# Optimization experiments

Measured on AMD Instinct MI355X. Metric: run time of the kernel, lower is better.

## Reference

```python
import jax, jax.numpy as jnp
import numpy as np

B, C, H, W = 8, 256, 64, 64
HEADS, HID = 8, 64
TMP = HEADS * HID  # 512


def setup_inputs() -> dict:
    key = jax.random.key(0)
    ks = jax.random.split(key, 6)
    s = lambda fan: 1.0 / np.sqrt(fan)
    fmap = jax.random.normal(ks[0], (B, C, H, W), jnp.float32)
    Wq = jax.random.normal(ks[1], (TMP, C), jnp.float32) * s(C)          # to_q 1x1 conv (no bias)
    Wdw = jax.random.normal(ks[2], (C, 1, 3, 3), jnp.float32) * s(9)     # depthwise 3x3 (groups=C, no bias)
    Wkv = jax.random.normal(ks[3], (2 * TMP, C), jnp.float32) * s(C)     # 1x1 conv producing k,v (no bias)
    Wout = jax.random.normal(ks[4], (C, TMP), jnp.float32) * s(TMP)      # to_out 1x1 conv
    bout = jax.random.normal(ks[5], (C,), jnp.float32) * 0.01
    return {"fmap": fmap, "Wq": Wq, "Wdw": Wdw, "Wkv": Wkv, "Wout": Wout, "bout": bout}


def reference(fmap, Wq, Wdw, Wkv, Wout, bout):
    heads, hid = HEADS, HID
    scale = hid ** (-0.5)
    b, c, h, w = fmap.shape
    n = h * w

    # 1x1 conv == channel GEMM
    q = jnp.einsum('bcxy,oc->boxy', fmap, Wq)
    # depthwise 3x3, padding=1
    dw = jax.lax.conv_general_dilated(
        fmap, Wdw, window_strides=(1, 1), padding='SAME',
        dimension_numbers=('NCHW', 'OIHW', 'NCHW'), feature_group_count=c)
    kv = jnp.einsum('bcxy,oc->boxy', dw, Wkv)
    k, v = jnp.split(kv, 2, axis=1)

    # 'b (h c) x y -> b h (x y) c'
    def to_seq(t):
        return t.reshape(b, heads, hid, n).transpose(0, 1, 3, 2)  # [b, h, n, d]

    q, k, v = to_seq(q), to_seq(k), to_seq(v)
    q = jax.nn.softmax(q, axis=-1) * scale   # softmax over feature dim
    k = jax.nn.softmax(k, axis=-2)           # softmax over token dim

    ctx = jnp.einsum('bhnd,bhne->bhde', k, v)    # [b, h, d, d]
    out = jnp.einsum('bhnd,bhde->bhne', q, ctx)  # [b, h, n, d]

    # '(b h) (x y) d -> b (h d) x y'
    out = out.transpose(0, 1, 3, 2).reshape(b, heads * hid, h, w)

    # to_out: GELU (exact) then 1x1 conv with bias (mode='ac')
    out = jax.nn.gelu(out, approximate=False)
    return jnp.einsum('bcxy,oc->boxy', out, Wout) + bout[None, :, None, None]
```

## Files before the change

kernel.cpp:

```cpp
#include <hip/hip_runtime.h>
#include <hip/hip_bf16.h>
#include <math.h>

#define Bx 8
#define Cc 256
#define Nn 4096
#define TMPc 512

typedef unsigned short ushort;
typedef unsigned int uint;
typedef unsigned long long ull;
typedef __attribute__((ext_vector_type(8))) short bf16x8;
typedef __attribute__((ext_vector_type(4))) float f32x4;

union F4 { float4 v; float f[4]; };

__device__ __forceinline__ ushort f2bf(float x) {
  uint u = __float_as_uint(x);
  uint r = (u + 0x7fffu + ((u >> 16) & 1u)) >> 16;
  return (ushort)r;
}
__device__ __forceinline__ float gelu_fast(float x) {
  float u = 0.70710678118654752f * x;
  float au = fabsf(u);
  float t = __builtin_amdgcn_rcpf(1.0f + 0.3275911f * au);
  float poly = ((((1.061405429f * t - 1.453152027f) * t + 1.421413741f) * t -
                 0.284496736f) * t + 0.254829592f) * t;
  float e = 1.0f - poly * __expf(-u * u);
  float erfu = copysignf(e, u);
  return 0.5f * x * (1.0f + erfu);
}

typedef const __attribute__((address_space(1))) uint* gp1_t;
typedef __attribute__((address_space(3))) uint* lp3_t;
__device__ __forceinline__ void gload16(void* lds, const void* g) {
  __builtin_amdgcn_global_load_lds((gp1_t)g, (lp3_t)lds, 16, 0, 0);
}
__device__ __forceinline__ bf16x8 fragread(const char* lds, int row, int kc) {
  return *(const bf16x8*)(lds + row * 64 + ((kc ^ (row & 3)) << 4));
}
__device__ __forceinline__ void stage2(char* buf, const ushort* src, int ld,
                                       int row0, int col, int w, int prow, int gst) {
  int off = __builtin_amdgcn_readfirstlane(w * 2048);
  gload16(buf + off, src + (size_t)(row0 + prow) * ld + col + gst * 8);
  gload16(buf + off + 1024, src + (size_t)(row0 + 16 + prow) * ld + col + gst * 8);
}

#define CGRP 32
__global__ __launch_bounds__(256) void convfuse_k(const float* __restrict__ fmap,
                                                  const float* __restrict__ Wdw,
                                                  ushort* __restrict__ fmapT,
                                                  ushort* __restrict__ dwT) {
  __shared__ float sin_[CGRP][6 * 64 + 1];
  __shared__ float wl[CGRP][9];
  int t = threadIdx.x;
  int y0 = blockIdx.x * 4;
  int c0 = blockIdx.y * CGRP;
  int z = blockIdx.z;
  for (int i = t; i < CGRP * 9; i += 256) wl[i / 9][i % 9] = Wdw[c0 * 9 + i];
  const float* src = fmap + ((size_t)z * Cc + c0) * 4096;
#pragma unroll
  for (int it = 0; it < 12; ++it) {
    int idx = it * 256 + t;
    int c = idx / 96, rem = idx % 96, yy = rem >> 4, x4 = rem & 15;
    int gy = y0 - 1 + yy;
    F4 v;
    if ((unsigned)gy < 64u)
      v.v = *(const float4*)&src[(size_t)c * 4096 + gy * 64 + x4 * 4];
    else
      v.f[0] = v.f[1] = v.f[2] = v.f[3] = 0.f;
#pragma unroll
    for (int j = 0; j < 4; ++j) sin_[c][yy * 64 + x4 * 4 + j] = v.f[j];
  }
  __syncthreads();
  int c8 = (t & 3) * 8;
  int nl = t >> 2;
  size_t nbase = (size_t)z * 4096 + (size_t)y0 * 64;
#pragma unroll
  for (int it = 0; it < 4; ++it) {
    int n = it * 64 + nl;
    int y = n >> 6, x = n & 63;
    union { ushort u[8]; uint4 q; } fo, go;
#pragma unroll
    for (int cc = 0; cc < 8; ++cc) {
      int c = c8 + cc;
      fo.u[cc] = f2bf(sin_[c][(y + 1) * 64 + x]);
      float acc = 0.f;
#pragma unroll
      for (int dy = 0; dy < 3; ++dy) {
#pragma unroll
        for (int dx = 0; dx < 3; ++dx) {
          int xx = x + dx - 1;
          float pv = ((unsigned)xx < 64u) ? sin_[c][(y + dy) * 64 + xx] : 0.f;
          acc += pv * wl[c][dy * 3 + dx];
        }
      }
      go.u[cc] = f2bf(acc);
    }
    *(uint4*)&fmapT[(nbase + n) * Cc + c0 + c8] = fo.q;
    *(uint4*)&dwT[(nbase + n) * Cc + c0 + c8] = go.q;
  }
}

__global__ __launch_bounds__(256) void cvtb3_k(const float* __restrict__ Wq,
                                               const float* __restrict__ Wkv,
                                               const float* __restrict__ Wout,
                                               ushort* __restrict__ WqB,
                                               ushort* __restrict__ WkvB,
                                               ushort* __restrict__ WoutB) {
  int i = blockIdx.x * 256 + threadIdx.x;
  const float* s;
  ushort* d;
  int idx;
  if (i < 32768) { s = Wq; d = WqB; idx = i; }
  else if (i < 98304) { s = Wkv; d = WkvB; idx = i - 32768; }
  else { s = Wout; d = WoutB; idx = i - 98304; }
  F4 v; v.v = *(const float4*)&s[(size_t)idx * 4];
  union { ushort u[4]; uint2 q; } o;
#pragma unroll
  for (int j = 0; j < 4; ++j) o.u[j] = f2bf(v.f[j]);
  *(uint2*)&d[(size_t)idx * 4] = o.q;
}

__global__ __launch_bounds__(256, 2) void kvgemm3_k(const ushort* __restrict__ WkvB,
                                                    const ushort* __restrict__ dwT,
                                                    ushort* __restrict__ kv) {
  __shared__ __align__(16) char lds[57344];
  char* Bres = lds;
  char* Asg  = lds + 32768;
  int t = threadIdx.x, w = t >> 6, l = t & 63;
  int z = blockIdx.y, n0 = blockIdx.x * 64;
  int rl = l & 15, kc = l >> 4;
  int prow = l >> 2;
  int gst = (l & 3) ^ ((l >> 2) & 3);

  const ushort* dT = dwT + ((size_t)z * 4096 + n0) * 256;
#pragma unroll
  for (int p = 0; p < 8; ++p) {
    int row = (w * 8 + p) * 2 + (l >> 5);
    int cs = l & 31;
    int off = __builtin_amdgcn_readfirstlane((w * 8 + p) * 1024);
    gload16(Bres + off, dT + (size_t)row * 256 + ((cs ^ (row & 7)) * 8));
  }
  stage2(Asg, WkvB, 256, w * 32, 0, w, prow, gst);
  stage2(Asg + 8192, WkvB, 256, w * 32, 32, w, prow, gst);
  asm volatile("s_waitcnt vmcnt(0)" ::: "memory");
  __syncthreads();

  ushort* kz = kv + (size_t)z * 1024 * 4096;
#pragma unroll
  for (int c = 0; c < 8; ++c) {
    f32x4 acc[2][4];
#pragma unroll
    for (int i = 0; i < 2; ++i)
#pragma unroll
      for (int j = 0; j < 4; ++j) acc[i][j] = (f32x4){0.f, 0.f, 0.f, 0.f};
#pragma unroll
    for (int k0 = 0; k0 < 8; ++k0) {
      int s = c * 8 + k0;
      if (s + 2 < 64) {
        int s2 = s + 2;
        stage2(Asg + (s2 % 3) * 8192, WkvB, 256, (s2 >> 3) * 128 + w * 32,
               (s2 & 7) * 32, w, prow, gst);
      }
      if (s < 62) asm volatile("s_waitcnt vmcnt(4)" ::: "memory");
      else if (s == 62) asm volatile("s_waitcnt vmcnt(2)" ::: "memory");
      else asm volatile("s_waitcnt vmcnt(0)" ::: "memory");
      const char* bp = Asg + (s % 3) * 8192 + w * 2048;
      bf16x8 a0 = fragread(bp, rl, kc);
      bf16x8 a1 = fragread(bp, 16 + rl, kc);
#pragma unroll
      for (int j = 0; j < 4; ++j) {
        int n = 16 * j + rl;
        bf16x8 b = *(const bf16x8*)(Bres + n * 512 + (((k0 * 4 + kc) ^ (n & 7)) << 4));
        acc[0][j] = __builtin_amdgcn_mfma_f32_16x16x32_bf16(a0, b, acc[0][j], 0, 0, 0);
        acc[1][j] = __builtin_amdgcn_mfma_f32_16x16x32_bf16(a1, b, acc[1][j], 0, 0, 0);
      }
    }
#pragma unroll
    for (int i = 0; i < 2; ++i) {
#pragma unroll
      for (int reg = 0; reg < 4; ++reg) {
        int r = c * 128 + w * 32 + 16 * i + 4 * kc + reg;
#pragma unroll
        for (int j = 0; j < 4; ++j) {
          int col = n0 + 16 * j + rl;
          float v = acc[i][j][reg];
          kz[(size_t)r * 4096 + col] = f2bf(c < 4 ? __expf(v) : v);
        }
      }
    }
  }
}

__global__ __launch_bounds__(256) void ctx_mfma(const ushort* __restrict__ kv,
                                                float* __restrict__ ctxf,
                                                float* __restrict__ sf) {
  __shared__ __align__(16) char lds[8192];
  int t = threadIdx.x, w = t >> 6, l = t & 63;
  int s = blockIdx.x;
  int h = blockIdx.y & 7, z = blockIdx.y >> 3;
  const ushort* kb = kv + ((size_t)z * 1024 + h * 64) * 4096;
  const ushort* vb = kv + ((size_t)z * 1024 + 512 + h * 64) * 4096;
  f32x4 acc[2][2];
  f32x4 accs[2];
#pragma unroll
  for (int i = 0; i < 2; ++i) {
    accs[i] = (f32x4){0.f, 0.f, 0.f, 0.f};
#pragma unroll
    for (int j = 0; j < 2; ++j) acc[i][j] = (f32x4){0.f, 0.f, 0.f, 0.f};
  }
  bf16x8 ones;
#pragma unroll
  for (int i = 0; i < 8; ++i) ones[i] = (short)0x3F80;
  int wr = (w >> 1) * 32, wc = (w & 1) * 32;
  int rl = l & 15, kc = l >> 4;
  int srow = (l >> 2) & 15, scol = l & 3;
  for (int it = 0; it < 16; ++it) {
    int k0 = s * 512 + it * 32;
    __syncthreads();
    {
      int row = w * 16 + srow;
      int g = scol ^ (row & 3);
      int off = __builtin_amdgcn_readfirstlane(w * 1024);
      gload16(lds + off, vb + (size_t)row * 4096 + k0 + g * 8);
      gload16(lds + 4096 + off, kb + (size_t)row * 4096 + k0 + g * 8);
    }
    asm volatile("s_waitcnt vmcnt(0)" ::: "memory");
    __syncthreads();
    bf16x8 a[2], b[2];
#pragma unroll
    for (int i = 0; i < 2; ++i) a[i] = fragread(lds, wr + i * 16 + rl, kc);
#pragma unroll
    for (int i = 0; i < 2; ++i) b[i] = fragread(lds + 4096, wc + i * 16 + rl, kc);
#pragma unroll
    for (int i = 0; i < 2; ++i)
#pragma unroll
      for (int j = 0; j < 2; ++j)
        acc[i][j] = __builtin_amdgcn_mfma_f32_16x16x32_bf16(a[i], b[j], acc[i][j], 0, 0, 0);
    if (w < 2) {
#pragma unroll
      for (int j = 0; j < 2; ++j)
        accs[j] = __builtin_amdgcn_mfma_f32_16x16x32_bf16(b[j], ones, accs[j], 0, 0, 0);
    }
  }
  float* cf = ctxf + (size_t)(z * 8 + h) * 4096;
#pragma unroll
  for (int i = 0; i < 2; ++i)
#pragma unroll
    for (int reg = 0; reg < 4; ++reg) {
      int e = wr + i * 16 + kc * 4 + reg;
#pragma unroll
      for (int j = 0; j < 2; ++j) {
        int d = wc + j * 16 + rl;
        atomicAdd(&cf[e * 64 + d], acc[i][j][reg]);
      }
    }
  if (w < 2 && rl == 0) {
    float* sp = sf + (size_t)(z * 8 + h) * 64;
#pragma unroll
    for (int j = 0; j < 2; ++j)
#pragma unroll
      for (int reg = 0; reg < 4; ++reg)
        atomicAdd(&sp[wc + j * 16 + kc * 4 + reg], accs[j][reg]);
  }
}

__global__ __launch_bounds__(256) void ctx_cvt(const float* __restrict__ ctxf,
                                               const float* __restrict__ sf,
                                               ushort* __restrict__ ctxb) {
  int page = blockIdx.x;
  const float* s = ctxf + (size_t)page * 4096;
  const float* sp = sf + (size_t)page * 64;
  ushort* d = ctxb + (size_t)page * 4096;
  int t = threadIdx.x;
  int e = t >> 2, d0 = (t & 3) * 16;
  union { ushort u[16]; uint4 q[2]; } o;
#pragma unroll
  for (int j = 0; j < 16; ++j) {
    int dd = d0 + j;
    o.u[j] = f2bf(s[e * 64 + dd] / sp[dd]);
  }
  uint4* dp = (uint4*)&d[e * 64 + d0];
  dp[0] = o.q[0]; dp[1] = o.q[1];
}

__global__ __launch_bounds__(256, 2) void qao_k(const ushort* __restrict__ fmapT,
                                                const ushort* __restrict__ WqB,
                                                const ushort* __restrict__ ctxb,
                                                const ushort* __restrict__ WoutB,
                                                const float* __restrict__ bout,
                                                float* __restrict__ out) {
  __shared__ __align__(16) char lds[73728];
  __shared__ float wsum[4][64];
  char* qbuf = lds;
  char* Bres = lds + 16384;
  char* Asg  = lds + 49152;
  int t = threadIdx.x, w = t >> 6, l = t & 63;
  int z = blockIdx.y, n0 = blockIdx.x * 64;
  int rl = l & 15, kc = l >> 4;
  int prow = l >> 2;
  int gst = (l & 3) ^ ((l >> 2) & 3);
  int hh = w >> 1;
  int wcn = (w & 1) * 32;

  const ushort* fT = fmapT + ((size_t)z * 4096 + n0) * 256;
#pragma unroll
  for (int p = 0; p < 8; ++p) {
    int row = (w * 8 + p) * 2 + (l >> 5);
    int cs = l & 31;
    int off = __builtin_amdgcn_readfirstlane((w * 8 + p) * 1024);
    gload16(Bres + off, fT + (size_t)row * 256 + ((cs ^ (row & 7)) * 8));
  }
  stage2(Asg, WqB, 256, w * 32, 0, w, prow, gst);
  stage2(Asg + 8192, WqB, 256, w * 32, 32, w, prow, gst);

  f32x4 oacc[4][4];
#pragma unroll
  for (int i = 0; i < 4; ++i)
#pragma unroll
    for (int j = 0; j < 4; ++j) oacc[i][j] = (f32x4){0.f, 0.f, 0.f, 0.f};

  asm volatile("s_waitcnt vmcnt(0)" ::: "memory");
  __syncthreads();

  for (int c = 0; c < 4; ++c) {
    const ushort* Wqc = WqB + (size_t)(c * 128) * 256;
    f32x4 qa[2][4];
#pragma unroll
    for (int i = 0; i < 2; ++i)
#pragma unroll
      for (int j = 0; j < 4; ++j) qa[i][j] = (f32x4){0.f, 0.f, 0.f, 0.f};
#pragma unroll
    for (int k0 = 0; k0 < 8; ++k0) {
      if (k0 + 2 < 8)
        stage2(Asg + ((k0 + 2) % 3) * 8192, Wqc, 256, w * 32, (k0 + 2) * 32, w, prow, gst);
      if (k0 < 6) asm volatile("s_waitcnt vmcnt(4)" ::: "memory");
      else if (k0 == 6) asm volatile("s_waitcnt vmcnt(2)" ::: "memory");
      else asm volatile("s_waitcnt vmcnt(0)" ::: "memory");
      const char* bp = Asg + (k0 % 3) * 8192 + w * 2048;
      bf16x8 a0 = fragread(bp, rl, kc);
      bf16x8 a1 = fragread(bp, 16 + rl, kc);
#pragma unroll
      for (int j = 0; j < 4; ++j) {
        int n = 16 * j + rl;
        bf16x8 b = *(const bf16x8*)(Bres + n * 512 + (((k0 * 4 + kc) ^ (n & 7)) << 4));
        qa[0][j] = __builtin_amdgcn_mfma_f32_16x16x32_bf16(a0, b, qa[0][j], 0, 0, 0);
        qa[1][j] = __builtin_amdgcn_mfma_f32_16x16x32_bf16(a1, b, qa[1][j], 0, 0, 0);
      }
    }
    const ushort* cpg = ctxb + (size_t)(z * 8 + c * 2 + hh) * 4096;
    bf16x8 ca[2][4];
#pragma unroll
    for (int s2 = 0; s2 < 2; ++s2)
#pragma unroll
      for (int i = 0; i < 4; ++i)
        ca[s2][i] = *(const bf16x8*)(cpg + (size_t)(16 * i + rl) * 64 + s2 * 32 + kc * 8);
    float sj[4];
#pragma unroll
    for (int j = 0; j < 4; ++j) {
      float s = 0.f;
#pragma unroll
      for (int i = 0; i < 2; ++i)
#pragma unroll
        for (int reg = 0; reg < 4; ++reg) {
          float e = __expf(qa[i][j][reg]);
          qa[i][j][reg] = e;
          s += e;
        }
      s += __shfl_xor(s, 16, 64);
      s += __shfl_xor(s, 32, 64);
      sj[j] = s;
    }
    if (l < 16) {
#pragma unroll
      for (int j = 0; j < 4; ++j) wsum[w][j * 16 + l] = sj[j];
    }
    __syncthreads();
#pragma unroll
    for (int j = 0; j < 4; ++j) {
      float tot = wsum[w][16 * j + rl] + wsum[w ^ 1][16 * j + rl];
      float inv = 0.125f / tot;
#pragma unroll
      for (int i = 0; i < 2; ++i)
#pragma unroll
        for (int reg = 0; reg < 4; ++reg) qa[i][j][reg] *= inv;
    }
#pragma unroll
    for (int i = 0; i < 2; ++i)
#pragma unroll
      for (int j = 0; j < 4; ++j) {
        int n = 16 * j + rl;
        int dby = (w * 32 + 16 * i + 4 * kc) * 2;
        union { ushort u[4]; ull q; } pk;
#pragma unroll
        for (int reg = 0; reg < 4; ++reg) pk.u[reg] = f2bf(qa[i][j][reg]);
        *(ull*)(qbuf + n * 256 + (dby ^ ((n & 7) << 4))) = pk.q;
      }
    __syncthreads();
    f32x4 pacc[4][2];
#pragma unroll
    for (int i = 0; i < 4; ++i)
#pragma unroll
      for (int j = 0; j < 2; ++j) pacc[i][j] = (f32x4){0.f, 0.f, 0.f, 0.f};
#pragma unroll
    for (int s2 = 0; s2 < 2; ++s2) {
      bf16x8 pb[2];
#pragma unroll
      for (int j = 0; j < 2; ++j) {
        int n = wcn + 16 * j + rl;
        int dby = hh * 128 + s2 * 64 + kc * 16;
        pb[j] = *(const bf16x8*)(qbuf + n * 256 + (dby ^ ((n & 7) << 4)));
      }
#pragma unroll
      for (int i = 0; i < 4; ++i)
#pragma unroll
        for (int j = 0; j < 2; ++j)
          pacc[i][j] = __builtin_amdgcn_mfma_f32_16x16x32_bf16(ca[s2][i], pb[j], pacc[i][j], 0, 0, 0);
    }
#pragma unroll
    for (int i = 0; i < 4; ++i)
#pragma unroll
      for (int j = 0; j < 2; ++j) {
        int n = wcn + 16 * j + rl;
        int mby = (hh * 64 + 16 * i + 4 * kc) * 2;
        union { ushort u[4]; ull q; } pk;
#pragma unroll
        for (int reg = 0; reg < 4; ++reg) pk.u[reg] = f2bf(gelu_fast(pacc[i][j][reg]));
        *(ull*)(qbuf + n * 256 + (mby ^ ((n & 7) << 4))) = pk.q;
      }
    __syncthreads();
    stage2(Asg, WoutB, 512, w * 64, c * 128, w, prow, gst);
    stage2(Asg + 8192, WoutB, 512, w * 64 + 32, c * 128, w, prow, gst);
    bf16x8 ob[4];
#pragma unroll
    for (int s = 0; s < 8; ++s) {
      if (s + 2 < 8) {
        int s2 = s + 2;
        stage2(Asg + (s2 % 3) * 8192, WoutB, 512, w * 64 + (s2 & 1) * 32,
               c * 128 + (s2 >> 1) * 32, w, prow, gst);
      }
      if (s < 6) asm volatile("s_waitcnt vmcnt(4)" ::: "memory");
      else if (s == 6) asm volatile("s_waitcnt vmcnt(2)" ::: "memory");
      else asm volatile("s_waitcnt vmcnt(0)" ::: "memory");
      int half = s & 1, ks = s >> 1;
      if (half == 0) {
#pragma unroll
        for (int j = 0; j < 4; ++j) {
          int n = 16 * j + rl;
          ob[j] = *(const bf16x8*)(qbuf + n * 256 + ((ks * 64 + kc * 16) ^ ((n & 7) << 4)));
        }
      }
      const char* bp = Asg + (s % 3) * 8192 + w * 2048;
      bf16x8 a0 = fragread(bp, rl, kc);
      bf16x8 a1 = fragread(bp, 16 + rl, kc);
#pragma unroll
      for (int j = 0; j < 4; ++j) {
        oacc[half * 2][j] = __builtin_amdgcn_mfma_f32_16x16x32_bf16(a0, ob[j], oacc[half * 2][j], 0, 0, 0);
        oacc[half * 2 + 1][j] = __builtin_amdgcn_mfma_f32_16x16x32_bf16(a1, ob[j], oacc[half * 2 + 1][j], 0, 0, 0);
      }
    }
    if (c < 3) {
      const ushort* Wqn = WqB + (size_t)((c + 1) * 128) * 256;
      stage2(Asg, Wqn, 256, w * 32, 0, w, prow, gst);
      stage2(Asg + 8192, Wqn, 256, w * 32, 32, w, prow, gst);
    }
  }
  float* oz = out + (size_t)z * Cc * Nn + n0;
#pragma unroll
  for (int i = 0; i < 4; ++i) {
#pragma unroll
    for (int reg = 0; reg < 4; ++reg) {
      int crow = w * 64 + 16 * i + 4 * kc + reg;
      float bv = bout[crow];
      float* rowp = oz + (size_t)crow * 4096;
#pragma unroll
      for (int j = 0; j < 4; ++j) rowp[16 * j + rl] = oacc[i][j][reg] + bv;
    }
  }
}

extern "C" void kernel_launch(void* const* d_in, const int* in_sizes, int n_in,
                              void* d_out, int out_size, void* d_ws, size_t ws_size,
                              hipStream_t stream) {
  (void)in_sizes; (void)n_in; (void)out_size; (void)ws_size;
  const float* fmap = (const float*)d_in[0];
  const float* Wq   = (const float*)d_in[1];
  const float* Wdw  = (const float*)d_in[2];
  const float* Wkv  = (const float*)d_in[3];
  const float* Wout = (const float*)d_in[4];
  const float* bout = (const float*)d_in[5];
  float* out = (float*)d_out;

  ushort* WqB   = (ushort*)d_ws;
  ushort* WkvB  = WqB + 512 * 256;
  ushort* WoutB = WkvB + 1024 * 256;
  ushort* fmapT = WoutB + 256 * 512;
  ushort* dwT   = fmapT + (size_t)Bx * 4096 * 256;
  ushort* kv    = dwT + (size_t)Bx * 4096 * 256;
  ushort* ctxb  = kv + (size_t)Bx * 1024 * 4096;
  float*  ctxf  = (float*)(ctxb + (size_t)Bx * 8 * 4096);
  float*  sf    = ctxf + (size_t)Bx * 8 * 64 * 64;

  cvtb3_k<<<dim3(512), 256, 0, stream>>>(Wq, Wkv, Wout, WqB, WkvB, WoutB);
  convfuse_k<<<dim3(16, Cc / CGRP, Bx), 256, 0, stream>>>(fmap, Wdw, fmapT, dwT);
  kvgemm3_k<<<dim3(64, Bx), 256, 0, stream>>>(WkvB, dwT, kv);
  hipMemsetAsync(ctxf, 0, (size_t)Bx * 8 * (4096 + 64) * sizeof(float), stream);
  ctx_mfma<<<dim3(8, Bx * 8), 256, 0, stream>>>(kv, ctxf, sf);
  ctx_cvt<<<dim3(Bx * 8), 256, 0, stream>>>(ctxf, sf, ctxb);
  qao_k<<<dim3(64, Bx), 256, 0, stream>>>(fmapT, WqB, ctxb, WoutB, bout, out);
}
```

Baseline: 122.4 us.

## Retile q/attention/out kernel to 32-token tiles with per-head loop for occupancy

The fused q-projection/attention/output kernel now processes 32 tokens per block instead of 64 and iterates over single heads rather than head pairs. That halves LDS use and accumulator registers so four blocks can share a CU, and the grid doubles to 128x8. It also adds lgkmcnt fences before LDS-overwriting async loads in the staging loops and moves the ctx memset to the start of the stream. In exchange, each block reloads the Wq and Wout weights for a smaller token tile, which raises weight traffic, and the per-head loop needs more barriers.

```diff
diff --git a/kernel.cpp b/kernel.cpp
--- a/kernel.cpp
+++ b/kernel.cpp
@@ -36,8 +36,16 @@
 __device__ __forceinline__ void gload16(void* lds, const void* g) {
   __builtin_amdgcn_global_load_lds((gp1_t)g, (lp3_t)lds, 16, 0, 0);
 }
+__device__ __forceinline__ void lgkm_fence() {
+  asm volatile("s_waitcnt lgkmcnt(0)" ::: "memory");
+}
 __device__ __forceinline__ bf16x8 fragread(const char* lds, int row, int kc) {
   return *(const bf16x8*)(lds + row * 64 + ((kc ^ (row & 3)) << 4));
+}
+__device__ __forceinline__ void stage1(char* buf, const ushort* src, int ld,
+                                       int row0, int col, int w, int prow, int gst) {
+  int off = __builtin_amdgcn_readfirstlane(w * 1024);
+  gload16(buf + off, src + (size_t)(row0 + prow) * ld + col + gst * 8);
 }
 __device__ __forceinline__ void stage2(char* buf, const ushort* src, int ld,
                                        int row0, int col, int w, int prow, int gst) {
@@ -160,6 +168,7 @@
       int s = c * 8 + k0;
       if (s + 2 < 64) {
         int s2 = s + 2;
+        lgkm_fence();
         stage2(Asg + (s2 % 3) * 8192, WkvB, 256, (s2 >> 3) * 128 + w * 32,
                (s2 & 7) * 32, w, prow, gst);
       }
@@ -285,197 +294,182 @@
   dp[0] = o.q[0]; dp[1] = o.q[1];
 }
 
-__global__ __launch_bounds__(256, 2) void qao_k(const ushort* __restrict__ fmapT,
+__global__ __launch_bounds__(256, 4) void qao_k(const ushort* __restrict__ fmapT,
                                                 const ushort* __restrict__ WqB,
                                                 const ushort* __restrict__ ctxb,
                                                 const ushort* __restrict__ WoutB,
                                                 const float* __restrict__ bout,
                                                 float* __restrict__ out) {
-  __shared__ __align__(16) char lds[73728];
-  __shared__ float wsum[4][64];
-  char* qbuf = lds;
-  char* Bres = lds + 16384;
-  char* Asg  = lds + 49152;
+  __shared__ __align__(16) char lds[36864];
+  __shared__ float wsum[4][32];
+  char* Bres = lds;
+  char* qB   = lds + 16384;
+  char* gB   = lds + 20480;
+  char* Asg  = lds + 24576;
   int t = threadIdx.x, w = t >> 6, l = t & 63;
-  int z = blockIdx.y, n0 = blockIdx.x * 64;
+  int z = blockIdx.y, n0 = blockIdx.x * 32;
   int rl = l & 15, kc = l >> 4;
   int prow = l >> 2;
   int gst = (l & 3) ^ ((l >> 2) & 3);
-  int hh = w >> 1;
-  int wcn = (w & 1) * 32;
+  int erow0 = w * 16;
+  int orow0 = w * 64;
 
   const ushort* fT = fmapT + ((size_t)z * 4096 + n0) * 256;
 #pragma unroll
-  for (int p = 0; p < 8; ++p) {
-    int row = (w * 8 + p) * 2 + (l >> 5);
+  for (int p = 0; p < 4; ++p) {
+    int row = (w * 4 + p) * 2 + (l >> 5);
     int cs = l & 31;
-    int off = __builtin_amdgcn_readfirstlane((w * 8 + p) * 1024);
+    int off = __builtin_amdgcn_readfirstlane((w * 4 + p) * 1024);
     gload16(Bres + off, fT + (size_t)row * 256 + ((cs ^ (row & 7)) * 8));
   }
-  stage2(Asg, WqB, 256, w * 32, 0, w, prow, gst);
-  stage2(Asg + 8192, WqB, 256, w * 32, 32, w, prow, gst);
-
-  f32x4 oacc[4][4];
-#pragma unroll
-  for (int i = 0; i < 4; ++i)
-#pragma unroll
-    for (int j = 0; j < 4; ++j) oacc[i][j] = (f32x4){0.f, 0.f, 0.f, 0.f};
+  stage1(Asg, WqB, 256, erow0, 0, w, prow, gst);
+  stage1(Asg + 4096, WqB, 256, erow0, 32, w, prow, gst);
+
+  f32x4 oacc[4][2];
+#pragma unroll
+  for (int g = 0; g < 4; ++g)
+#pragma unroll
+    for (int j = 0; j < 2; ++j) oacc[g][j] = (f32x4){0.f, 0.f, 0.f, 0.f};
 
   asm volatile("s_waitcnt vmcnt(0)" ::: "memory");
   __syncthreads();
 
-  for (int c = 0; c < 4; ++c) {
-    const ushort* Wqc = WqB + (size_t)(c * 128) * 256;
-    f32x4 qa[2][4];
-#pragma unroll
-    for (int i = 0; i < 2; ++i)
-#pragma unroll
-      for (int j = 0; j < 4; ++j) qa[i][j] = (f32x4){0.f, 0.f, 0.f, 0.f};
+  for (int h = 0; h < 8; ++h) {
+    const ushort* Wqc = WqB + (size_t)(h * 64) * 256;
+    f32x4 qa[2];
+#pragma unroll
+    for (int j = 0; j < 2; ++j) qa[j] = (f32x4){0.f, 0.f, 0.f, 0.f};
 #pragma unroll
     for (int k0 = 0; k0 < 8; ++k0) {
-      if (k0 + 2 < 8)
-        stage2(Asg + ((k0 + 2) % 3) * 8192, Wqc, 256, w * 32, (k0 + 2) * 32, w, prow, gst);
-      if (k0 < 6) asm volatile("s_waitcnt vmcnt(4)" ::: "memory");
-      else if (k0 == 6) asm volatile("s_waitcnt vmcnt(2)" ::: "memory");
+      if (k0 + 2 < 8) {
+        lgkm_fence();
+        stage1(Asg + ((k0 + 2) % 3) * 4096, Wqc, 256, erow0, (k0 + 2) * 32, w, prow, gst);
+      }
+      if (k0 < 6) asm volatile("s_waitcnt vmcnt(2)" ::: "memory");
+      else if (k0 == 6) asm volatile("s_waitcnt vmcnt(1)" ::: "memory");
       else asm volatile("s_waitcnt vmcnt(0)" ::: "memory");
-      const char* bp = Asg + (k0 % 3) * 8192 + w * 2048;
+      const char* bp = Asg + (k0 % 3) * 4096 + w * 1024;
       bf16x8 a0 = fragread(bp, rl, kc);
-      bf16x8 a1 = fragread(bp, 16 + rl, kc);
-#pragma unroll
-      for (int j = 0; j < 4; ++j) {
+#pragma unroll
+      for (int j = 0; j < 2; ++j) {
         int n = 16 * j + rl;
         bf16x8 b = *(const bf16x8*)(Bres + n * 512 + (((k0 * 4 + kc) ^ (n & 7)) << 4));
-        qa[0][j] = __builtin_amdgcn_mfma_f32_16x16x32_bf16(a0, b, qa[0][j], 0, 0, 0);
-        qa[1][j] = __builtin_amdgcn_mfma_f32_16x16x32_bf16(a1, b, qa[1][j], 0, 0, 0);
-      }
-    }
-    const ushort* cpg = ctxb + (size_t)(z * 8 + c * 2 + hh) * 4096;
-    bf16x8 ca[2][4];
+        qa[j] = __builtin_amdgcn_mfma_f32_16x16x32_bf16(a0, b, qa[j], 0, 0, 0);
+      }
+    }
+    const ushort* cpg = ctxb + (size_t)(z * 8 + h) * 4096;
+    bf16x8 ca[2];
 #pragma unroll
     for (int s2 = 0; s2 < 2; ++s2)
-#pragma unroll
-      for (int i = 0; i < 4; ++i)
-        ca[s2][i] = *(const bf16x8*)(cpg + (size_t)(16 * i + rl) * 64 + s2 * 32 + kc * 8);
-    float sj[4];
-#pragma unroll
-    for (int j = 0; j < 4; ++j) {
+      ca[s2] = *(const bf16x8*)(cpg + (size_t)(erow0 + rl) * 64 + s2 * 32 + kc * 8);
+    float sj[2];
+#pragma unroll
+    for (int j = 0; j < 2; ++j) {
       float s = 0.f;
 #pragma unroll
-      for (int i = 0; i < 2; ++i)
-#pragma unroll
-        for (int reg = 0; reg < 4; ++reg) {
-          float e = __expf(qa[i][j][reg]);
-          qa[i][j][reg] = e;
-          s += e;
-        }
+      for (int reg = 0; reg < 4; ++reg) {
+        float e = __expf(qa[j][reg]);
+        qa[j][reg] = e;
+        s += e;
+      }
       s += __shfl_xor(s, 16, 64);
       s += __shfl_xor(s, 32, 64);
       sj[j] = s;
     }
     if (l < 16) {
 #pragma unroll
-      for (int j = 0; j < 4; ++j) wsum[w][j * 16 + l] = sj[j];
+      for (int j = 0; j < 2; ++j) wsum[w][j * 16 + l] = sj[j];
     }
     __syncthreads();
 #pragma unroll
-    for (int j = 0; j < 4; ++j) {
-      float tot = wsum[w][16 * j + rl] + wsum[w ^ 1][16 * j + rl];
+    for (int j = 0; j < 2; ++j) {
+      float tot = wsum[0][16 * j + rl] + wsum[1][16 * j + rl] +
+                  wsum[2][16 * j + rl] + wsum[3][16 * j + rl];
       float inv = 0.125f / tot;
 #pragma unroll
-      for (int i = 0; i < 2; ++i)
-#pragma unroll
-        for (int reg = 0; reg < 4; ++reg) qa[i][j][reg] *= inv;
-    }
-#pragma unroll
-    for (int i = 0; i < 2; ++i)
-#pragma unroll
-      for (int j = 0; j < 4; ++j) {
-        int n = 16 * j + rl;
-        int dby = (w * 32 + 16 * i + 4 * kc) * 2;
-        union { ushort u[4]; ull q; } pk;
-#pragma unroll
-        for (int reg = 0; reg < 4; ++reg) pk.u[reg] = f2bf(qa[i][j][reg]);
-        *(ull*)(qbuf + n * 256 + (dby ^ ((n & 7) << 4))) = pk.q;
-      }
+      for (int reg = 0; reg < 4; ++reg) qa[j][reg] *= inv;
+    }
+#pragma unroll
+    for (int j = 0; j < 2; ++j) {
+      int n = 16 * j + rl;
+      int dby = (erow0 + 4 * kc) * 2;
+      union { ushort u[4]; ull q; } pk;
+#pragma unroll
+      for (int reg = 0; reg < 4; ++reg) pk.u[reg] = f2bf(qa[j][reg]);
+      *(ull*)(qB + n * 128 + (dby ^ ((n & 7) << 4))) = pk.q;
+    }
     __syncthreads();
-    f32x4 pacc[4][2];
-#pragma unroll
-    for (int i = 0; i < 4; ++i)
-#pragma unroll
-      for (int j = 0; j < 2; ++j) pacc[i][j] = (f32x4){0.f, 0.f, 0.f, 0.f};
+    f32x4 pacc[2];
+#pragma unroll
+    for (int j = 0; j < 2; ++j) pacc[j] = (f32x4){0.f, 0.f, 0.f, 0.f};
 #pragma unroll
     for (int s2 = 0; s2 < 2; ++s2) {
       bf16x8 pb[2];
 #pragma unroll
       for (int j = 0; j < 2; ++j) {
-        int n = wcn + 16 * j + rl;
-        int dby = hh * 128 + s2 * 64 + kc * 16;
-        pb[j] = *(const bf16x8*)(qbuf + n * 256 + (dby ^ ((n & 7) << 4)));
-      }
-#pragma unroll
-      for (int i = 0; i < 4; ++i)
-#pragma unroll
-        for (int j = 0; j < 2; ++j)
-          pacc[i][j] = __builtin_amdgcn_mfma_f32_16x16x32_bf16(ca[s2][i], pb[j], pacc[i][j], 0, 0, 0);
-    }
-#pragma unroll
-    for (int i = 0; i < 4; ++i)
-#pragma unroll
-      for (int j = 0; j < 2; ++j) {
-        int n = wcn + 16 * j + rl;
-        int mby = (hh * 64 + 16 * i + 4 * kc) * 2;
-        union { ushort u[4]; ull q; } pk;
-#pragma unroll
-        for (int reg = 0; reg < 4; ++reg) pk.u[reg] = f2bf(gelu_fast(pacc[i][j][reg]));
-        *(ull*)(qbuf + n * 256 + (mby ^ ((n & 7) << 4))) = pk.q;
-      }
+        int n = 16 * j + rl;
+        int dby = s2 * 64 + kc * 16;
+        pb[j] = *(const bf16x8*)(qB + n * 128 + (dby ^ ((n & 7) << 4)));
+      }
+#pragma unroll
+      for (int j = 0; j < 2; ++j)
+        pacc[j] = __builtin_amdgcn_mfma_f32_16x16x32_bf16(ca[s2], pb[j], pacc[j], 0, 0, 0);
+    }
+#pragma unroll
+    for (int j = 0; j < 2; ++j) {
+      int n = 16 * j + rl;
+      int eby = (erow0 + 4 * kc) * 2;
+      union { ushort u[4]; ull q; } pk;
+#pragma unroll
+      for (int reg = 0; reg < 4; ++reg) pk.u[reg] = f2bf(gelu_fast(pacc[j][reg]));
+      *(ull*)(gB + n * 128 + (eby ^ ((n & 7) << 4))) = pk.q;
+    }
     __syncthreads();
-    stage2(Asg, WoutB, 512, w * 64, c * 128, w, prow, gst);
-    stage2(Asg + 8192, WoutB, 512, w * 64 + 32, c * 128, w, prow, gst);
-    bf16x8 ob[4];
+    stage1(Asg, WoutB, 512, orow0, h * 64, w, prow, gst);
+    stage1(Asg + 4096, WoutB, 512, orow0 + 16, h * 64, w, prow, gst);
+    bf16x8 ob[2];
 #pragma unroll
     for (int s = 0; s < 8; ++s) {
       if (s + 2 < 8) {
-        int s2 = s + 2;
-        stage2(Asg + (s2 % 3) * 8192, WoutB, 512, w * 64 + (s2 & 1) * 32,
-               c * 128 + (s2 >> 1) * 32, w, prow, gst);
-      }
-      if (s < 6) asm volatile("s_waitcnt vmcnt(4)" ::: "memory");
-      else if (s == 6) asm volatile("s_waitcnt vmcnt(2)" ::: "memory");
+        int sn = s + 2;
+        lgkm_fence();
+        stage1(Asg + (sn % 3) * 4096, WoutB, 512, orow0 + (sn & 3) * 16,
+               h * 64 + (sn >> 2) * 32, w, prow, gst);
+      }
+      if (s < 6) asm volatile("s_waitcnt vmcnt(2)" ::: "memory");
+      else if (s == 6) asm volatile("s_waitcnt vmcnt(1)" ::: "memory");
       else asm volatile("s_waitcnt vmcnt(0)" ::: "memory");
-      int half = s & 1, ks = s >> 1;
-      if (half == 0) {
-#pragma unroll
-        for (int j = 0; j < 4; ++j) {
+      int g = s & 3, ks = s >> 2;
+      if (g == 0) {
+#pragma unroll
+        for (int j = 0; j < 2; ++j) {
           int n = 16 * j + rl;
-          ob[j] = *(const bf16x8*)(qbuf + n * 256 + ((ks * 64 + kc * 16) ^ ((n & 7) << 4)));
+          ob[j] = *(const bf16x8*)(gB + n * 128 + ((ks * 64 + kc * 16) ^ ((n & 7) << 4)));
         }
       }
-      const char* bp = Asg + (s % 3) * 8192 + w * 2048;
+      const char* bp = Asg + (s % 3) * 4096 + w * 1024;
       bf16x8 a0 = fragread(bp, rl, kc);
-      bf16x8 a1 = fragread(bp, 16 + rl, kc);
-#pragma unroll
-      for (int j = 0; j < 4; ++j) {
-        oacc[half * 2][j] = __builtin_amdgcn_mfma_f32_16x16x32_bf16(a0, ob[j], oacc[half * 2][j], 0, 0, 0);
-        oacc[half * 2 + 1][j] = __builtin_amdgcn_mfma_f32_16x16x32_bf16(a1, ob[j], oacc[half * 2 + 1][j], 0, 0, 0);
-      }
-    }
-    if (c < 3) {
-      const ushort* Wqn = WqB + (size_t)((c + 1) * 128) * 256;
-      stage2(Asg, Wqn, 256, w * 32, 0, w, prow, gst);
-      stage2(Asg + 8192, Wqn, 256, w * 32, 32, w, prow, gst);
+#pragma unroll
+      for (int j = 0; j < 2; ++j)
+        oacc[g][j] = __builtin_amdgcn_mfma_f32_16x16x32_bf16(a0, ob[j], oacc[g][j], 0, 0, 0);
+    }
+    if (h < 7) {
+      const ushort* Wqn = WqB + (size_t)((h + 1) * 64) * 256;
+      lgkm_fence();
+      stage1(Asg, Wqn, 256, erow0, 0, w, prow, gst);
+      stage1(Asg + 4096, Wqn, 256, erow0, 32, w, prow, gst);
     }
   }
   float* oz = out + (size_t)z * Cc * Nn + n0;
 #pragma unroll
-  for (int i = 0; i < 4; ++i) {
+  for (int g = 0; g < 4; ++g) {
 #pragma unroll
     for (int reg = 0; reg < 4; ++reg) {
-      int crow = w * 64 + 16 * i + 4 * kc + reg;
+      int crow = orow0 + g * 16 + 4 * kc + reg;
       float bv = bout[crow];
       float* rowp = oz + (size_t)crow * 4096;
 #pragma unroll
-      for (int j = 0; j < 4; ++j) rowp[16 * j + rl] = oacc[i][j][reg] + bv;
+      for (int j = 0; j < 2; ++j) rowp[16 * j + rl] = oacc[g][j][reg] + bv;
     }
   }
 }
@@ -502,11 +496,11 @@
   float*  ctxf  = (float*)(ctxb + (size_t)Bx * 8 * 4096);
   float*  sf    = ctxf + (size_t)Bx * 8 * 64 * 64;
 
+  hipMemsetAsync(ctxf, 0, (size_t)Bx * 8 * (4096 + 64) * sizeof(float), stream);
   cvtb3_k<<<dim3(512), 256, 0, stream>>>(Wq, Wkv, Wout, WqB, WkvB, WoutB);
   convfuse_k<<<dim3(16, Cc / CGRP, Bx), 256, 0, stream>>>(fmap, Wdw, fmapT, dwT);
   kvgemm3_k<<<dim3(64, Bx), 256, 0, stream>>>(WkvB, dwT, kv);
-  hipMemsetAsync(ctxf, 0, (size_t)Bx * 8 * (4096 + 64) * sizeof(float), stream);
   ctx_mfma<<<dim3(8, Bx * 8), 256, 0, stream>>>(kv, ctxf, sf);
   ctx_cvt<<<dim3(Bx * 8), 256, 0, stream>>>(ctxf, sf, ctxb);
-  qao_k<<<dim3(64, Bx), 256, 0, stream>>>(fmapT, WqB, ctxb, WoutB, bout, out);
-}
+  qao_k<<<dim3(128, Bx), 256, 0, stream>>>(fmapT, WqB, ctxb, WoutB, bout, out);
+}
```

New measurement: 128.4 us. 4.9% more time.

## Double-buffer ctx_mfma LDS loads and fence LDS reads before async stages

Applied to the files above, without the earlier changes.

ctx_mfma now uses two LDS buffers so the global-to-LDS load of the next K/V chunk is issued before computing on the current one, with one barrier per iteration instead of two. Several stage2 calls in kvgemm and qao get an lgkmcnt(0) wait so pending LDS fragment reads finish before the async global_load_lds overwrites the ring slot, which is a correctness hazard fix that may add stalls. The memset is moved to the front of the launch sequence. The change doubles ctx_mfma shared memory in exchange for overlapping load latency with MFMA work.

```diff
diff --git a/kernel.cpp b/kernel.cpp
--- a/kernel.cpp
+++ b/kernel.cpp
@@ -35,6 +35,9 @@
 typedef __attribute__((address_space(3))) uint* lp3_t;
 __device__ __forceinline__ void gload16(void* lds, const void* g) {
   __builtin_amdgcn_global_load_lds((gp1_t)g, (lp3_t)lds, 16, 0, 0);
+}
+__device__ __forceinline__ void lgkm_fence() {
+  asm volatile("s_waitcnt lgkmcnt(0)" ::: "memory");
 }
 __device__ __forceinline__ bf16x8 fragread(const char* lds, int row, int kc) {
   return *(const bf16x8*)(lds + row * 64 + ((kc ^ (row & 3)) << 4));
@@ -160,6 +163,7 @@
       int s = c * 8 + k0;
       if (s + 2 < 64) {
         int s2 = s + 2;
+        lgkm_fence();
         stage2(Asg + (s2 % 3) * 8192, WkvB, 256, (s2 >> 3) * 128 + w * 32,
                (s2 & 7) * 32, w, prow, gst);
       }
@@ -196,7 +200,7 @@
 __global__ __launch_bounds__(256) void ctx_mfma(const ushort* __restrict__ kv,
                                                 float* __restrict__ ctxf,
                                                 float* __restrict__ sf) {
-  __shared__ __align__(16) char lds[8192];
+  __shared__ __align__(16) char lds[16384];
   int t = threadIdx.x, w = t >> 6, l = t & 63;
   int s = blockIdx.x;
   int h = blockIdx.y & 7, z = blockIdx.y >> 3;
@@ -216,23 +220,26 @@
   int wr = (w >> 1) * 32, wc = (w & 1) * 32;
   int rl = l & 15, kc = l >> 4;
   int srow = (l >> 2) & 15, scol = l & 3;
+  int row = w * 16 + srow;
+  int g = scol ^ (row & 3);
+  int soff = __builtin_amdgcn_readfirstlane(w * 1024);
+#define CSTG(bb, it)                                                      \
+  {                                                                       \
+    int k0_ = s * 512 + (it) * 32;                                        \
+    gload16(lds + (bb) + soff, vb + (size_t)row * 4096 + k0_ + g * 8);    \
+    gload16(lds + (bb) + 4096 + soff, kb + (size_t)row * 4096 + k0_ + g * 8); \
+  }
+  CSTG(0, 0);
+  asm volatile("s_waitcnt vmcnt(0)" ::: "memory");
+  __syncthreads();
   for (int it = 0; it < 16; ++it) {
-    int k0 = s * 512 + it * 32;
-    __syncthreads();
-    {
-      int row = w * 16 + srow;
-      int g = scol ^ (row & 3);
-      int off = __builtin_amdgcn_readfirstlane(w * 1024);
-      gload16(lds + off, vb + (size_t)row * 4096 + k0 + g * 8);
-      gload16(lds + 4096 + off, kb + (size_t)row * 4096 + k0 + g * 8);
-    }
-    asm volatile("s_waitcnt vmcnt(0)" ::: "memory");
-    __syncthreads();
+    int cur = (it & 1) << 13;
+    if (it + 1 < 16) CSTG(cur ^ 8192, it + 1);
     bf16x8 a[2], b[2];
 #pragma unroll
-    for (int i = 0; i < 2; ++i) a[i] = fragread(lds, wr + i * 16 + rl, kc);
-#pragma unroll
-    for (int i = 0; i < 2; ++i) b[i] = fragread(lds + 4096, wc + i * 16 + rl, kc);
+    for (int i = 0; i < 2; ++i) a[i] = fragread(lds + cur, wr + i * 16 + rl, kc);
+#pragma unroll
+    for (int i = 0; i < 2; ++i) b[i] = fragread(lds + cur + 4096, wc + i * 16 + rl, kc);
 #pragma unroll
     for (int i = 0; i < 2; ++i)
 #pragma unroll
@@ -243,6 +250,8 @@
       for (int j = 0; j < 2; ++j)
         accs[j] = __builtin_amdgcn_mfma_f32_16x16x32_bf16(b[j], ones, accs[j], 0, 0, 0);
     }
+    asm volatile("s_waitcnt vmcnt(0)" ::: "memory");
+    __syncthreads();
   }
   float* cf = ctxf + (size_t)(z * 8 + h) * 4096;
 #pragma unroll
@@ -264,6 +273,7 @@
       for (int reg = 0; reg < 4; ++reg)
         atomicAdd(&sp[wc + j * 16 + kc * 4 + reg], accs[j][reg]);
   }
+#undef CSTG
 }
 
 __global__ __launch_bounds__(256) void ctx_cvt(const float* __restrict__ ctxf,
@@ -333,8 +343,10 @@
       for (int j = 0; j < 4; ++j) qa[i][j] = (f32x4){0.f, 0.f, 0.f, 0.f};
 #pragma unroll
     for (int k0 = 0; k0 < 8; ++k0) {
-      if (k0 + 2 < 8)
+      if (k0 + 2 < 8) {
+        lgkm_fence();
         stage2(Asg + ((k0 + 2) % 3) * 8192, Wqc, 256, w * 32, (k0 + 2) * 32, w, prow, gst);
+      }
       if (k0 < 6) asm volatile("s_waitcnt vmcnt(4)" ::: "memory");
       else if (k0 == 6) asm volatile("s_waitcnt vmcnt(2)" ::: "memory");
       else asm volatile("s_waitcnt vmcnt(0)" ::: "memory");
@@ -437,6 +449,7 @@
     for (int s = 0; s < 8; ++s) {
       if (s + 2 < 8) {
         int s2 = s + 2;
+        lgkm_fence();
         stage2(Asg + (s2 % 3) * 8192, WoutB, 512, w * 64 + (s2 & 1) * 32,
                c * 128 + (s2 >> 1) * 32, w, prow, gst);
       }
@@ -462,6 +475,7 @@
     }
     if (c < 3) {
       const ushort* Wqn = WqB + (size_t)((c + 1) * 128) * 256;
+      lgkm_fence();
       stage2(Asg, Wqn, 256, w * 32, 0, w, prow, gst);
       stage2(Asg + 8192, Wqn, 256, w * 32, 32, w, prow, gst);
     }
@@ -502,10 +516,10 @@
   float*  ctxf  = (float*)(ctxb + (size_t)Bx * 8 * 4096);
   float*  sf    = ctxf + (size_t)Bx * 8 * 64 * 64;
 
+  hipMemsetAsync(ctxf, 0, (size_t)Bx * 8 * (4096 + 64) * sizeof(float), stream);
   cvtb3_k<<<dim3(512), 256, 0, stream>>>(Wq, Wkv, Wout, WqB, WkvB, WoutB);
   convfuse_k<<<dim3(16, Cc / CGRP, Bx), 256, 0, stream>>>(fmap, Wdw, fmapT, dwT);
   kvgemm3_k<<<dim3(64, Bx), 256, 0, stream>>>(WkvB, dwT, kv);
-  hipMemsetAsync(ctxf, 0, (size_t)Bx * 8 * (4096 + 64) * sizeof(float), stream);
   ctx_mfma<<<dim3(8, Bx * 8), 256, 0, stream>>>(kv, ctxf, sf);
   ctx_cvt<<<dim3(Bx * 8), 256, 0, stream>>>(ctxf, sf, ctxb);
   qao_k<<<dim3(64, Bx), 256, 0, stream>>>(fmapT, WqB, ctxb, WoutB, bout, out);
```

Result: no change. 121.4 us (-0.8%).
